# Performance work log

Measured on AMD Instinct MI355X. Metric: run time of the kernel, lower is better.

The kernel has to match this reference:

```python
import jax, jax.numpy as jnp
import numpy as np
from jax import lax

INPUT_SIZE = 512
THRESHOLD = 0.5
IOU_TH = 0.3
MAX_ROIS = 32   # py_cpu_nms(...)[:32]
ROI = 7
NEG = jnp.float32(-1e30)


def _make_anchors(fh, fw, stride):
    # 3 scales x 3 ratios = 9 anchors per cell, laid out in (h, w, anchor)
    # order to match permute(0,2,3,1).view(-1) of the conv heads.
    scales = np.array([32.0, 64.0, 128.0])
    ratios = np.array([0.5, 1.0, 2.0])
    ws = (scales[:, None] * np.sqrt(ratios)[None, :]).reshape(-1)
    hs = (scales[:, None] / np.sqrt(ratios)[None, :]).reshape(-1)
    cy = (np.arange(fh) + 0.5) * stride
    cx = (np.arange(fw) + 0.5) * stride
    CX, CY = np.meshgrid(cx, cy)
    CX = CX[..., None]; CY = CY[..., None]
    a = np.stack([CX - ws / 2, CY - hs / 2, CX + ws / 2, CY + hs / 2], axis=-1)
    return jnp.asarray(a.reshape(-1, 4), jnp.float32)


def setup_inputs() -> dict:
    key = jax.random.key(0)
    k1, k2, k3 = jax.random.split(key, 3)
    B, C, FH, FW, A, stride = 4, 256, 64, 64, 9, 8
    featureMap = jax.random.normal(k1, (B, C, FH, FW), jnp.float32)
    # small init so sigmoid scores spread across threshold and exp(tw) stays sane
    w_cls = jax.random.normal(k2, (A, C, 3, 3), jnp.float32) * 0.05
    w_loc = jax.random.normal(k3, (4 * A, C, 3, 3), jnp.float32) * 0.01
    prior_anchor = _make_anchors(FH, FW, stride)
    return {"featureMap": featureMap, "prior_anchor": prior_anchor,
            "w_cls": w_cls, "w_loc": w_loc, "stride": stride}


def _conv(x, w):
    return lax.conv_general_dilated(x, w, (1, 1), "SAME",
                                    dimension_numbers=("NCHW", "OIHW", "NCHW"))


def _decode(loc, anchors):
    aw = anchors[:, 2] - anchors[:, 0]
    ah = anchors[:, 3] - anchors[:, 1]
    acx = anchors[:, 0] + 0.5 * aw
    acy = anchors[:, 1] + 0.5 * ah
    cx = acx + loc[:, 0] * aw
    cy = acy + loc[:, 1] * ah
    w = aw * jnp.exp(loc[:, 2])
    h = ah * jnp.exp(loc[:, 3])
    return jnp.stack([cx - 0.5 * w, cy - 0.5 * h, cx + 0.5 * w, cy + 0.5 * h], axis=1)


def _iou_one(box, boxes):
    xx1 = jnp.maximum(box[0], boxes[:, 0]); yy1 = jnp.maximum(box[1], boxes[:, 1])
    xx2 = jnp.minimum(box[2], boxes[:, 2]); yy2 = jnp.minimum(box[3], boxes[:, 3])
    inter = jnp.clip(xx2 - xx1, 0) * jnp.clip(yy2 - yy1, 0)
    a1 = (box[2] - box[0]) * (box[3] - box[1])
    a2 = (boxes[:, 2] - boxes[:, 0]) * (boxes[:, 3] - boxes[:, 1])
    return inter / (a1 + a2 - inter + 1e-9)


def _nms(boxes, scores, valid):
    # greedy NMS, fixed MAX_ROIS rounds (== sort-by-score py_cpu_nms + [:32])
    N = scores.shape[0]
    s0 = jnp.where(valid, scores, -1.0)

    def body(i, carry):
        s, picks, ok = carry
        idx = jnp.argmax(s)
        good = s[idx] > 0.0
        picks = picks.at[i].set(idx.astype(jnp.int32))
        ok = ok.at[i].set(good)
        sup = (_iou_one(boxes[idx], boxes) > IOU_TH) | (jnp.arange(N) == idx)
        return (jnp.where(sup, -1.0, s), picks, ok)

    _, picks, ok = lax.fori_loop(
        0, MAX_ROIS, body,
        (s0, jnp.zeros(MAX_ROIS, jnp.int32), jnp.zeros(MAX_ROIS, bool)))
    return picks, ok


def _ceil_div(a, b):
    return -(-a // b)


def _adaptive_maxpool(feat, box):
    # feat: [C, FH, FW]; box: int32 [x1, y1, x2, y2] in feature-map coords.
    # Faithful F.adaptive_max_pool2d bins: start=floor(i*h/7), end=ceil((i+1)*h/7).
    FH, FW = feat.shape[1], feat.shape[2]
    x1, y1, x2, y2 = box[0], box[1], box[2], box[3]
    h = y2 - y1; w = x2 - x1
    i = jnp.arange(ROI)
    rs = y1 + (i * h) // ROI; re = y1 + _ceil_div((i + 1) * h, ROI)
    cs = x1 + (i * w) // ROI; ce = x1 + _ceil_div((i + 1) * w, ROI)
    hh = jnp.arange(FH); ww = jnp.arange(FW)
    rm = jnp.where((hh >= rs[:, None]) & (hh < re[:, None]), 0.0, NEG)  # [7, FH]
    cm = jnp.where((ww >= cs[:, None]) & (ww < ce[:, None]), 0.0, NEG)  # [7, FW]
    t = jnp.max(feat[None] + rm[:, None, :, None], axis=2)              # [7, C, FW]
    out = jnp.max(t[:, None] + cm[None, :, None, :], axis=3)            # [7, 7, C]
    return jnp.transpose(out, (2, 0, 1))                                # [C, 7, 7]


def reference(featureMap, prior_anchor, w_cls, w_loc, stride):
    B, C, FH, FW = featureMap.shape
    cls = jax.nn.sigmoid(_conv(featureMap, w_cls))                      # [B, A, FH, FW]
    cls = jnp.transpose(cls, (0, 2, 3, 1)).reshape(B, -1)               # [B, N]
    loc = jnp.transpose(_conv(featureMap, w_loc), (0, 2, 3, 1)).reshape(B, -1, 4)
    boxes = jax.vmap(_decode, in_axes=(0, None))(loc, prior_anchor)     # [B, N, 4]
    boxes = jnp.clip(boxes, 0.0, float(INPUT_SIZE))                     # clamp(0, input_size)
    valid = (cls > THRESHOLD) \
          & (boxes[..., 2] - boxes[..., 0] >= 2 * stride) \
          & (boxes[..., 3] - boxes[..., 1] >= 2 * stride)
    picks, ok = jax.vmap(_nms)(boxes, cls, valid)                       # [B, 32]
    sel_boxes = jnp.take_along_axis(boxes, picks[..., None], axis=1)    # [B, 32, 4]
    sel_scores = jnp.take_along_axis(cls, picks, axis=1)                # [B, 32]
    eval_boxes = jnp.where(
        ok[..., None],
        jnp.concatenate([sel_boxes, sel_scores[..., None]], axis=-1), 0.0)
    # src_coordinate.int() / stride -> integer feature-map coords
    ib = sel_boxes.astype(jnp.int32) // stride
    fx1 = jnp.clip(ib[..., 0], 0, FW - 1); fy1 = jnp.clip(ib[..., 1], 0, FH - 1)
    fx2 = jnp.clip(ib[..., 2], fx1 + 1, FW); fy2 = jnp.clip(ib[..., 3], fy1 + 1, FH)
    fb = jnp.stack([fx1, fy1, fx2, fy2], axis=-1).reshape(-1, 4)        # [B*32, 4]
    img = jnp.repeat(jnp.arange(B), MAX_ROIS)
    rois = lax.map(lambda a: _adaptive_maxpool(featureMap[a[1]], a[0]), (fb, img))
    rois = jnp.where(ok.reshape(-1)[:, None, None, None], rois, 0.0)    # [B*32, 256, 7, 7]
    return eval_boxes, ok, rois
```

## Files before the change

kernel.cpp:

```cpp
#include <hip/hip_runtime.h>
#include <hip/hip_bf16.h>

#define FHH 64
#define FWW 64
#define CIN 256
#define NB 4
#define NA 9
#define NANCH 36864
#define NPOS 4096
#define OC_TOTAL 45
#define OCP 48
#define MAXROIS 32
#define ROI 7
#define NEGV -1e30f
#define NCHUNK 576
#define NTH 16
#define CAP 1024

typedef unsigned long long u64;

__device__ __constant__ const float TH_LADDER[NTH] = {
    0.9999f, 0.9998f, 0.9995f, 0.999f, 0.998f, 0.997f, 0.995f, 0.993f,
    0.99f, 0.987f, 0.984f, 0.98f, 0.975f, 0.97f, 0.96f, 0.0f};

__global__ __launch_bounds__(256) void wtrans_kernel(
    const float* __restrict__ wcls,
    const float* __restrict__ wloc,
    float* __restrict__ wT,
    int* __restrict__ gcnt)
{
    if (blockIdx.x == 0 && threadIdx.x < NB * NTH) gcnt[threadIdx.x] = 0;
    int idx = blockIdx.x * 256 + threadIdx.x;
    int o = idx % 48;
    int rest = idx / 48;
    int tap = rest % 9;
    int c = rest / 9;
    float v = 0.f;
    if (o < OC_TOTAL) {
        v = (o < NA) ? wcls[((size_t)o * CIN + c) * 9 + tap]
                     : wloc[((size_t)(o - NA) * CIN + c) * 9 + tap];
    }
    wT[idx] = v;
}

__global__ __launch_bounds__(256) void conv_kernel(
    const float* __restrict__ feat,
    const float* __restrict__ wT,
    float* __restrict__ partial,
    int nkg, int cpk)
{
    __shared__ float flds[16][18][20];

    int blk = blockIdx.x;
    int low = blk & 7;
    int rest = blk >> 3;
    int kg = rest % nkg;
    int uhi = rest / nkg;
    int unit = uhi * 8 + low;
    int b = unit >> 4;
    int tile = unit & 15;

    int ty0 = (tile >> 2) * 16;
    int tx0 = (tile & 3) * 16;

    int pb = threadIdx.x & 63;
    int q = __builtin_amdgcn_readfirstlane(threadIdx.x >> 6);
    int ry0 = (pb >> 3) * 2;
    int rx0 = (pb & 7) * 2;

    int cbase = kg * cpk;

    float acc[2][2][12];
#pragma unroll
    for (int py = 0; py < 2; ++py)
#pragma unroll
        for (int px = 0; px < 2; ++px)
#pragma unroll
            for (int o = 0; o < 12; ++o) acc[py][px][o] = 0.f;

    for (int c0 = 0; c0 < cpk; c0 += 16) {
        __syncthreads();
        for (int idx = threadIdx.x; idx < 16 * 324; idx += 256) {
            int c = idx / 324;
            int r = idx - c * 324;
            int y = r / 18;
            int x = r - y * 18;
            int gy = ty0 + y - 1;
            int gx = tx0 + x - 1;
            float v = 0.f;
            if ((unsigned)gy < FHH && (unsigned)gx < FWW)
                v = feat[((size_t)(b * CIN + cbase + c0 + c) * FHH + gy) * FWW + gx];
            flds[c][y][x] = v;
        }
        __syncthreads();

        const float* wq = wT + (size_t)(cbase + c0) * 432 + q * 12;
        for (int c = 0; c < 16; ++c) {
            float f[4][4];
#pragma unroll
            for (int r = 0; r < 4; ++r) {
                float2 a0 = *(const float2*)&flds[c][ry0 + r][rx0];
                float2 a1 = *(const float2*)&flds[c][ry0 + r][rx0 + 2];
                f[r][0] = a0.x; f[r][1] = a0.y; f[r][2] = a1.x; f[r][3] = a1.y;
            }
#pragma unroll
            for (int tap = 0; tap < 9; ++tap) {
                int dy = tap / 3, dx = tap % 3;
                const float* wp = wq + (c * 9 + tap) * 48;
                float w[12];
#pragma unroll
                for (int o = 0; o < 12; ++o) w[o] = wp[o];
#pragma unroll
                for (int py = 0; py < 2; ++py)
#pragma unroll
                for (int px = 0; px < 2; ++px) {
                    float fv = f[py + dy][px + dx];
#pragma unroll
                    for (int o = 0; o < 12; ++o)
                        acc[py][px][o] += fv * w[o];
                }
            }
        }
    }

    float* pout = partial + ((size_t)kg * NB + b) * OCP * NPOS;
#pragma unroll
    for (int o = 0; o < 12; ++o) {
        int oo = q * 12 + o;
        float* op = pout + (size_t)oo * NPOS;
#pragma unroll
        for (int py = 0; py < 2; ++py)
#pragma unroll
        for (int px = 0; px < 2; ++px) {
            int pos = (ty0 + ry0 + py) * FWW + (tx0 + rx0 + px);
            op[pos] = acc[py][px][o];
        }
    }
}

__global__ __launch_bounds__(256) void decode_kernel(
    const float* __restrict__ partial,
    const float* __restrict__ anchors,
    const int* __restrict__ stridep,
    float* __restrict__ boxes,
    float* __restrict__ scores,
    int* __restrict__ gcnt,
    int nkg)
{
    __shared__ int hcnt[NTH];
    if (threadIdx.x < NTH) hcnt[threadIdx.x] = 0;
    __syncthreads();

    int t = blockIdx.x * 256 + threadIdx.x;
    int pos = t & (NPOS - 1);
    int ba = t >> 12;
    int b = ba / 9;
    int a = ba - b * 9;

    float cls = 0.f, l0 = 0.f, l1 = 0.f, l2 = 0.f, l3 = 0.f;
    for (int kg = 0; kg < nkg; ++kg) {
        const float* pk = partial + ((size_t)kg * NB + b) * OCP * NPOS;
        cls += pk[(size_t)a * NPOS + pos];
        l0 += pk[(size_t)(NA + a * 4 + 0) * NPOS + pos];
        l1 += pk[(size_t)(NA + a * 4 + 1) * NPOS + pos];
        l2 += pk[(size_t)(NA + a * 4 + 2) * NPOS + pos];
        l3 += pk[(size_t)(NA + a * 4 + 3) * NPOS + pos];
    }

    float sig = 1.f / (1.f + expf(-cls));
    int n = pos * NA + a;
    const float* an = anchors + (size_t)n * 4;
    float ax1 = an[0], ay1 = an[1], ax2 = an[2], ay2 = an[3];
    float aw = ax2 - ax1, ah = ay2 - ay1;
    float acx = ax1 + 0.5f * aw, acy = ay1 + 0.5f * ah;
    float cx = acx + l0 * aw;
    float cy = acy + l1 * ah;
    float w = aw * expf(l2);
    float h = ah * expf(l3);
    float x1 = fminf(fmaxf(cx - 0.5f * w, 0.f), 512.f);
    float y1 = fminf(fmaxf(cy - 0.5f * h, 0.f), 512.f);
    float x2 = fminf(fmaxf(cx + 0.5f * w, 0.f), 512.f);
    float y2 = fminf(fmaxf(cy + 0.5f * h, 0.f), 512.f);
    int stride = stridep[0];
    float msz = 2.f * (float)stride;
    bool valid = (sig > 0.5f) && ((x2 - x1) >= msz) && ((y2 - y1) >= msz);
    ((float4*)boxes)[(size_t)b * NANCH + n] = make_float4(x1, y1, x2, y2);
    scores[(size_t)b * NANCH + n] = valid ? sig : -1.0f;

#pragma unroll
    for (int i = 0; i < NTH; ++i) {
        u64 mb = __ballot(valid && sig >= TH_LADDER[i]);
        if ((threadIdx.x & 63) == 0 && mb)
            atomicAdd(&hcnt[i], (int)__popcll(mb));
    }
    __syncthreads();
    if (threadIdx.x < NTH && hcnt[threadIdx.x])
        atomicAdd(&gcnt[b * NTH + threadIdx.x], hcnt[threadIdx.x]);
}

__global__ __launch_bounds__(64) void choose_kernel(
    const int* __restrict__ gcnt,
    float* __restrict__ Tsel, int* __restrict__ Csel, int* __restrict__ Vsel,
    int* __restrict__ force, int* __restrict__ gcount, int cap)
{
    int b = threadIdx.x;
    if (b >= NB) return;
    int bestc = 0; float bt = TH_LADDER[0];
    for (int i = 0; i < NTH; ++i) {
        int c = gcnt[b * NTH + i];
        if (c <= cap && c > bestc) { bestc = c; bt = TH_LADDER[i]; }
    }
    int frc = (gcnt[b * NTH + 0] > cap) ? 1 : 0;
    if (frc) { bestc = cap; bt = TH_LADDER[0]; }
    Tsel[b] = bt; Csel[b] = bestc; Vsel[b] = gcnt[b * NTH + NTH - 1];
    force[b] = frc; gcount[b] = 0;
}

__global__ __launch_bounds__(256) void nms_compact_kernel(
    const float* __restrict__ scores,
    const float* __restrict__ Tsel,
    int* __restrict__ gcount,
    u64* __restrict__ candkey,
    int cap)
{
    __shared__ int lcnt;
    __shared__ int wbase[4];
    __shared__ int gbase;
    int t = blockIdx.x * 256 + threadIdx.x;
    int b = t / NANCH;
    int j = t - b * NANCH;
    int lane = threadIdx.x & 63;
    int w = threadIdx.x >> 6;
    if (threadIdx.x == 0) lcnt = 0;
    __syncthreads();
    float v = scores[t];
    float T = Tsel[b];
    bool p = (v > 0.f) && (v >= T);
    u64 m = __ballot(p);
    int cnt = (int)__popcll(m);
    if (lane == 0) wbase[w] = atomicAdd(&lcnt, cnt);
    __syncthreads();
    if (threadIdx.x == 0) gbase = lcnt ? atomicAdd(&gcount[b], lcnt) : 0;
    __syncthreads();
    if (p) {
        int off = (int)__popcll(m & ((1ULL << lane) - 1ULL));
        int slot = gbase + wbase[w] + off;
        if (slot < cap)
            candkey[(size_t)b * cap + slot] =
                ((u64)__float_as_uint(v) << 32) | (unsigned int)(~j);
    }
}

__device__ __forceinline__ void write_outputs(
    int b, int i, bool okv, int idx, float sc,
    const float4* Bb4, const int* stridep,
    float* d_out, int* ifb, int* iok)
{
    float4 bb = Bb4[idx];
    float* eb = d_out + ((size_t)b * MAXROIS + i) * 5;
    eb[0] = okv ? bb.x : 0.f;
    eb[1] = okv ? bb.y : 0.f;
    eb[2] = okv ? bb.z : 0.f;
    eb[3] = okv ? bb.w : 0.f;
    eb[4] = okv ? sc : 0.f;
    d_out[NB * MAXROIS * 5 + b * MAXROIS + i] = okv ? 1.f : 0.f;
    int st = stridep[0];
    int fx1 = min(max(((int)bb.x) / st, 0), FWW - 1);
    int fy1 = min(max(((int)bb.y) / st, 0), FHH - 1);
    int fx2 = min(max(((int)bb.z) / st, fx1 + 1), FWW);
    int fy2 = min(max(((int)bb.w) / st, fy1 + 1), FHH);
    int r = b * MAXROIS + i;
    ifb[r * 4 + 0] = fx1;
    ifb[r * 4 + 1] = fy1;
    ifb[r * 4 + 2] = fx2;
    ifb[r * 4 + 3] = fy2;
    iok[r] = okv ? 1 : 0;
}

__global__ __launch_bounds__(512) void nms_sortscan_kernel(
    const u64* __restrict__ candkey,
    const float* __restrict__ boxes,
    const int* __restrict__ Csel, const int* __restrict__ Vsel,
    const int* __restrict__ force,
    const int* __restrict__ stridep,
    float* __restrict__ d_out,
    int* __restrict__ ifb, int* __restrict__ iok, int* __restrict__ flag,
    int cap)
{
    __shared__ u64 skey[CAP];
    __shared__ float4 box_l[CAP];
    __shared__ u64 mask[CAP / 64];
    __shared__ int picks[MAXROIS];
    __shared__ int np_sh;

    int b = blockIdx.x;
    int tid = threadIdx.x;
    int lane = tid & 63;
    int C = Csel[b];
    if (tid == 0) np_sh = 0;

    int CSZ = 64;
    while (CSZ < C) CSZ <<= 1;

    for (int j = tid; j < CSZ; j += 512)
        skey[j] = (j < C) ? candkey[(size_t)b * cap + j] : 0ULL;

    int prev_cross = 1;
    for (int kk = 2; kk <= CSZ; kk <<= 1) {
        for (int jj = kk >> 1; jj > 0; jj >>= 1) {
            int cross = (jj >= 128) ? 1 : 0;
            if (cross || prev_cross) __syncthreads();
            for (int tt = tid; tt < (CSZ >> 1); tt += 512) {
                int i = ((tt & ~(jj - 1)) << 1) | (tt & (jj - 1));
                int l = i + jj;
                u64 a = skey[i], c2 = skey[l];
                bool up = ((i & kk) == 0);
                bool sw = up ? (a < c2) : (a > c2);
                if (sw) { skey[i] = c2; skey[l] = a; }
            }
            prev_cross = cross;
        }
    }
    __syncthreads();

    const float4* Bb4 = (const float4*)(boxes + (size_t)b * NANCH * 4);
    for (int j = tid; j < C; j += 512) {
        int id = (int)(~((unsigned int)(skey[j] & 0xFFFFFFFFULL)));
        box_l[j] = Bb4[id];
    }
    if (tid < CAP / 64) {
        int base = tid * 64;
        u64 m0;
        if (base >= C) m0 = ~0ULL;
        else if (base + 64 > C) m0 = ~((1ULL << (C - base)) - 1ULL);
        else m0 = 0ULL;
        mask[tid] = m0;
    }
    __syncthreads();

    for (int round = 0; round < MAXROIS; ++round) {
        u64 mw = (lane < CAP / 64) ? mask[lane] : ~0ULL;
        int bpos = __ffsll((u64)(~mw));
        int cand = bpos ? lane * 64 + bpos - 1 : 0x7FFFFFFF;
#pragma unroll
        for (int off = 32; off >= 1; off >>= 1)
            cand = min(cand, __shfl_xor(cand, off));
        int pj = cand;
        if (pj == 0x7FFFFFFF) break;
        if (tid == 0) {
            picks[round] = pj;
            np_sh = round + 1;
            atomicOr(&mask[pj >> 6], 1ULL << (pj & 63));
        }
        float4 pb = box_l[pj];
        float parea = (pb.z - pb.x) * (pb.w - pb.y);
        int j0 = tid * 2;
        u64 curm = mask[tid >> 5];
        u64 addm = 0ULL;
#pragma unroll
        for (int d = 0; d < 2; ++d) {
            int j = j0 + d;
            if (j > pj && j < C && !((curm >> (j & 63)) & 1ULL)) {
                float4 bb2 = box_l[j];
                float xx1 = fmaxf(pb.x, bb2.x), yy1 = fmaxf(pb.y, bb2.y);
                float xx2 = fminf(pb.z, bb2.z), yy2 = fminf(pb.w, bb2.w);
                float inter = fmaxf(xx2 - xx1, 0.f) * fmaxf(yy2 - yy1, 0.f);
                float a2 = (bb2.z - bb2.x) * (bb2.w - bb2.y);
                float iou = inter / (parea + a2 - inter + 1e-9f);
                if (iou > 0.3f) addm |= 1ULL << (j & 63);
            }
        }
        if (addm) atomicOr(&mask[tid >> 5], addm);
        __syncthreads();
    }
    __syncthreads();

    int np = np_sh;
    bool need_fb = force[b] || (np < MAXROIS && Vsel[b] > C);
    if (tid == 0) flag[b] = need_fb ? 1 : 0;
    if (!need_fb && tid < MAXROIS) {
        int i = tid;
        bool okv = i < np;
        int slot = okv ? picks[i] : 0;
        u64 k = skey[slot];
        int idx = okv ? (int)(~((unsigned int)(k & 0xFFFFFFFFULL))) : 0;
        float sc = okv ? __uint_as_float((unsigned int)(k >> 32)) : 0.f;
        write_outputs(b, i, okv, idx, sc, Bb4, stridep, d_out, ifb, iok);
    }
}

__global__ __launch_bounds__(1024) void nms_fallback_kernel(
    const float* __restrict__ boxes,
    const float* __restrict__ scores,
    const int* __restrict__ stridep,
    float* __restrict__ d_out,
    int* __restrict__ ifb,
    int* __restrict__ iok,
    const int* __restrict__ flag)
{
    __shared__ float s[NANCH];
    __shared__ float2 cmax[NCHUNK];
    __shared__ int   picks_sh[MAXROIS];
    __shared__ float pscore_sh[MAXROIS];

    int b = blockIdx.x;
    if (flag[b] == 0) return;

    const float4* Bb4 = (const float4*)(boxes + (size_t)b * NANCH * 4);
    const float* Sb = scores + (size_t)b * NANCH;
    int lane = threadIdx.x & 63;
    int w = threadIdx.x >> 6;

    for (int k = 0; k < 36; ++k) {
        int ch = w * 36 + k;
        int j = ch * 64 + lane;
        float v = Sb[j];
        s[j] = v;
        float bv = v; int bi = j;
#pragma unroll
        for (int off = 32; off >= 1; off >>= 1) {
            float ov = __shfl_xor(bv, off);
            int   oi = __shfl_xor(bi, off);
            if (ov > bv || (ov == bv && oi < bi)) { bv = ov; bi = oi; }
        }
        if (lane == 0) cmax[ch] = make_float2(bv, __int_as_float(bi));
    }
    __syncthreads();
    if (w != 0) return;

    float px1 = 0.f, py1 = 0.f, px2 = 0.f, py2 = 0.f, parea = 0.f;
    int np = 0;
    while (np < MAXROIS) {
        float bv = -2.f; int bi = 0x7fffffff;
#pragma unroll
        for (int k = 0; k < 9; ++k) {
            float2 cm = cmax[lane * 9 + k];
            int ci = __float_as_int(cm.y);
            if (cm.x > bv || (cm.x == bv && ci < bi)) { bv = cm.x; bi = ci; }
        }
#pragma unroll
        for (int off = 32; off >= 1; off >>= 1) {
            float ov = __shfl_xor(bv, off);
            int   oi = __shfl_xor(bi, off);
            if (ov > bv || (ov == bv && oi < bi)) { bv = ov; bi = oi; }
        }
        if (bv <= 0.f) break;
        int fi = bi; float fs = bv;

        float4 cbb = Bb4[fi];

        bool sup = false;
        if (lane < np) {
            float xx1 = fmaxf(px1, cbb.x), yy1 = fmaxf(py1, cbb.y);
            float xx2 = fminf(px2, cbb.z), yy2 = fminf(py2, cbb.w);
            float inter = fmaxf(xx2 - xx1, 0.f) * fmaxf(yy2 - yy1, 0.f);
            float a2 = (cbb.z - cbb.x) * (cbb.w - cbb.y);
            float iou = inter / (parea + a2 - inter + 1e-9f);
            sup = iou > 0.3f;
        }
        u64 m = __ballot(sup);

        int ch = fi >> 6;
        int j = ch * 64 + lane;
        float sv = (j == fi) ? -1.f : s[j];
        if (j == fi) s[j] = -1.f;
        float nv = sv; int ni = j;
#pragma unroll
        for (int off = 32; off >= 1; off >>= 1) {
            float ov = __shfl_xor(nv, off);
            int   oi = __shfl_xor(ni, off);
            if (ov > nv || (ov == nv && oi < ni)) { nv = ov; ni = oi; }
        }
        if (lane == 0) cmax[ch] = make_float2(nv, __int_as_float(ni));

        if (m == 0ULL) {
            if (lane == np) {
                px1 = cbb.x; py1 = cbb.y; px2 = cbb.z; py2 = cbb.w;
                parea = (px2 - px1) * (py2 - py1);
            }
            picks_sh[np] = fi;
            pscore_sh[np] = fs;
            ++np;
        }
    }

    if (lane < MAXROIS) {
        int i = lane;
        bool okv = i < np;
        int idx = okv ? picks_sh[i] : 0;
        float sc = okv ? pscore_sh[i] : 0.f;
        write_outputs(b, i, okv, idx, sc, Bb4, stridep, d_out, ifb, iok);
    }
}

__global__ __launch_bounds__(256) void roi_kernel(
    const float* __restrict__ feat,
    const int* __restrict__ ifb,
    const int* __restrict__ iok,
    float* __restrict__ out_rois)
{
    int t = blockIdx.x * 256 + threadIdx.x;
    int bin = t % 49;
    int rc = t / 49;
    int c = rc & 255;
    int r = rc >> 8;
    int i = bin / 7;
    int j = bin - i * 7;

    if (!iok[r]) { out_rois[t] = 0.f; return; }

    int x1 = ifb[r * 4 + 0];
    int y1 = ifb[r * 4 + 1];
    int x2 = ifb[r * 4 + 2];
    int y2 = ifb[r * 4 + 3];
    int h = y2 - y1;
    int w = x2 - x1;
    int b = r >> 5;

    int rs = y1 + (i * h) / ROI;
    int re = y1 + ((i + 1) * h + ROI - 1) / ROI;
    int cs = x1 + (j * w) / ROI;
    int ce = x1 + ((j + 1) * w + ROI - 1) / ROI;

    const float* F = feat + (size_t)(b * CIN + c) * NPOS;
    float m = NEGV;
    for (int y = rs; y < re; ++y) {
        const float* row = F + y * FWW;
        for (int x = cs; x < ce; ++x) m = fmaxf(m, row[x]);
    }
    out_rois[t] = m;
}

extern "C" void kernel_launch(void* const* d_in, const int* in_sizes, int n_in,
                              void* d_out, int out_size, void* d_ws, size_t ws_size,
                              hipStream_t stream) {
    const float* feat    = (const float*)d_in[0];
    const float* anchors = (const float*)d_in[1];
    const float* wcls    = (const float*)d_in[2];
    const float* wloc    = (const float*)d_in[3];
    const int*   stridep = (const int*)d_in[4];
    float* out = (float*)d_out;
    float* ws  = (float*)d_ws;

    const size_t P1 = (size_t)NB * OCP * NPOS;
    const size_t WTN = 256 * 9 * 48;
    const int cap = CAP;

    auto need = [&](int nk) -> size_t {
        size_t f = P1 * nk
                 + 589824 + 147456 + WTN
                 + (size_t)NB * cap * 2
                 + 2048;
        return f * 4;
    };
    int nkg = 16;
    if (ws_size < need(16)) {
        if (ws_size >= need(8)) { nkg = 8; }
        else { nkg = 4; }
    }

    float* partial   = ws;
    float* boxes     = partial + P1 * nkg;
    float* scores    = boxes + (size_t)NB * NANCH * 4;
    float* wT        = scores + (size_t)NB * NANCH;
    u64*   candkey   = (u64*)(wT + WTN);
    float* tailf     = (float*)(candkey + (size_t)NB * cap);
    int*   ifb       = (int*)tailf;
    int*   iok       = ifb + 512;
    int*   flag      = iok + 128;
    int*   gcnt      = flag + 4;
    float* Tsel      = (float*)(gcnt + 64);
    int*   Csel      = (int*)(Tsel + 4);
    int*   Vsel      = Csel + 4;
    int*   force     = Vsel + 4;
    int*   gcount    = force + 4;

    wtrans_kernel<<<432, 256, 0, stream>>>(wcls, wloc, wT, gcnt);
    conv_kernel<<<64 * nkg, 256, 0, stream>>>(feat, wT, partial, nkg, CIN / nkg);
    decode_kernel<<<(NB * NANCH) / 256, 256, 0, stream>>>(partial, anchors, stridep, boxes, scores, gcnt, nkg);
    choose_kernel<<<1, 64, 0, stream>>>(gcnt, Tsel, Csel, Vsel, force, gcount, cap);
    nms_compact_kernel<<<(NB * NANCH) / 256, 256, 0, stream>>>(scores, Tsel, gcount, candkey, cap);
    nms_sortscan_kernel<<<NB, 512, 0, stream>>>(candkey, boxes, Csel, Vsel, force, stridep, out, ifb, iok, flag, cap);
    nms_fallback_kernel<<<NB, 1024, 0, stream>>>(boxes, scores, stridep, out, ifb, iok, flag);
    roi_kernel<<<(NB * MAXROIS * CIN * 49) / 256, 256, 0, stream>>>(feat, ifb, iok, out + NB * MAXROIS * 5 + NB * MAXROIS);
}
```

Before: 140.1 us.

## Enlarge conv register tile to 2x4 and stage weights in LDS

The conv kernel now gives each thread a 2x4 pixel block (tiles of 16x32 instead of 16x16) and loads 8 channels per stage, with the weight slice for those channels copied into shared memory as float4s instead of read from global memory per tap. Outputs are written with float4 stores. The aim is more FMA per shared and global load and fewer weight fetches, at the cost of more accumulator registers and half as many blocks launched.

```diff
diff --git a/kernel.cpp b/kernel.cpp
--- a/kernel.cpp
+++ b/kernel.cpp
@@ -49,7 +49,8 @@
     float* __restrict__ partial,
     int nkg, int cpk)
 {
-    __shared__ float flds[16][18][20];
+    __shared__ float flds[8][18][40];
+    __shared__ float wlds[8][9][48];
 
     int blk = blockIdx.x;
     int low = blk & 7;
@@ -57,34 +58,33 @@
     int kg = rest % nkg;
     int uhi = rest / nkg;
     int unit = uhi * 8 + low;
-    int b = unit >> 4;
-    int tile = unit & 15;
-
-    int ty0 = (tile >> 2) * 16;
-    int tx0 = (tile & 3) * 16;
-
-    int pb = threadIdx.x & 63;
-    int q = __builtin_amdgcn_readfirstlane(threadIdx.x >> 6);
-    int ry0 = (pb >> 3) * 2;
-    int rx0 = (pb & 7) * 2;
+    int b = unit >> 3;
+    int tile = unit & 7;
+    int ty0 = (tile >> 1) * 16;
+    int tx0 = (tile & 1) * 32;
+
+    int slot = threadIdx.x & 63;
+    int q = threadIdx.x >> 6;
+    int ry0 = (slot >> 3) * 2;
+    int rx0 = (slot & 7) * 4;
 
     int cbase = kg * cpk;
 
-    float acc[2][2][12];
+    float acc[2][4][12];
 #pragma unroll
     for (int py = 0; py < 2; ++py)
 #pragma unroll
-        for (int px = 0; px < 2; ++px)
+        for (int px = 0; px < 4; ++px)
 #pragma unroll
             for (int o = 0; o < 12; ++o) acc[py][px][o] = 0.f;
 
-    for (int c0 = 0; c0 < cpk; c0 += 16) {
+    for (int c0 = 0; c0 < cpk; c0 += 8) {
         __syncthreads();
-        for (int idx = threadIdx.x; idx < 16 * 324; idx += 256) {
-            int c = idx / 324;
-            int r = idx - c * 324;
-            int y = r / 18;
-            int x = r - y * 18;
+        for (int idx = threadIdx.x; idx < 8 * 612; idx += 256) {
+            int c = idx / 612;
+            int r = idx - c * 612;
+            int y = r / 34;
+            int x = r - y * 34;
             int gy = ty0 + y - 1;
             int gx = tx0 + x - 1;
             float v = 0.f;
@@ -92,28 +92,38 @@
                 v = feat[((size_t)(b * CIN + cbase + c0 + c) * FHH + gy) * FWW + gx];
             flds[c][y][x] = v;
         }
+        {
+            const float4* src = (const float4*)(wT + (size_t)(cbase + c0) * 432);
+            float4* dst = (float4*)&wlds[0][0][0];
+            for (int idx = threadIdx.x; idx < 864; idx += 256)
+                dst[idx] = src[idx];
+        }
         __syncthreads();
 
-        const float* wq = wT + (size_t)(cbase + c0) * 432 + q * 12;
-        for (int c = 0; c < 16; ++c) {
-            float f[4][4];
+        for (int c = 0; c < 8; ++c) {
+            float f[4][6];
 #pragma unroll
             for (int r = 0; r < 4; ++r) {
                 float2 a0 = *(const float2*)&flds[c][ry0 + r][rx0];
                 float2 a1 = *(const float2*)&flds[c][ry0 + r][rx0 + 2];
-                f[r][0] = a0.x; f[r][1] = a0.y; f[r][2] = a1.x; f[r][3] = a1.y;
+                float2 a2 = *(const float2*)&flds[c][ry0 + r][rx0 + 4];
+                f[r][0] = a0.x; f[r][1] = a0.y; f[r][2] = a1.x;
+                f[r][3] = a1.y; f[r][4] = a2.x; f[r][5] = a2.y;
             }
 #pragma unroll
             for (int tap = 0; tap < 9; ++tap) {
-                int dy = tap / 3, dx = tap % 3;
-                const float* wp = wq + (c * 9 + tap) * 48;
-                float w[12];
-#pragma unroll
-                for (int o = 0; o < 12; ++o) w[o] = wp[o];
+                const int dy = tap / 3, dx = tap % 3;
+                const float* wp = &wlds[c][tap][q * 12];
+                float4 w0 = *(const float4*)(wp);
+                float4 w1 = *(const float4*)(wp + 4);
+                float4 w2 = *(const float4*)(wp + 8);
+                float w[12] = {w0.x, w0.y, w0.z, w0.w,
+                               w1.x, w1.y, w1.z, w1.w,
+                               w2.x, w2.y, w2.z, w2.w};
 #pragma unroll
                 for (int py = 0; py < 2; ++py)
 #pragma unroll
-                for (int px = 0; px < 2; ++px) {
+                for (int px = 0; px < 4; ++px) {
                     float fv = f[py + dy][px + dx];
 #pragma unroll
                     for (int o = 0; o < 12; ++o)
@@ -129,11 +139,12 @@
         int oo = q * 12 + o;
         float* op = pout + (size_t)oo * NPOS;
 #pragma unroll
-        for (int py = 0; py < 2; ++py)
-#pragma unroll
-        for (int px = 0; px < 2; ++px) {
-            int pos = (ty0 + ry0 + py) * FWW + (tx0 + rx0 + px);
-            op[pos] = acc[py][px][o];
+        for (int py = 0; py < 2; ++py) {
+            int row = ty0 + ry0 + py;
+            int col = tx0 + rx0;
+            float4 v = make_float4(acc[py][0][o], acc[py][1][o],
+                                   acc[py][2][o], acc[py][3][o]);
+            *(float4*)&op[row * FWW + col] = v;
         }
     }
 }
@@ -576,7 +587,7 @@
     int*   gcount    = force + 4;
 
     wtrans_kernel<<<432, 256, 0, stream>>>(wcls, wloc, wT, gcnt);
-    conv_kernel<<<64 * nkg, 256, 0, stream>>>(feat, wT, partial, nkg, CIN / nkg);
+    conv_kernel<<<32 * nkg, 256, 0, stream>>>(feat, wT, partial, nkg, CIN / nkg);
     decode_kernel<<<(NB * NANCH) / 256, 256, 0, stream>>>(partial, anchors, stridep, boxes, scores, gcnt, nkg);
     choose_kernel<<<1, 64, 0, stream>>>(gcnt, Tsel, Csel, Vsel, force, gcount, cap);
     nms_compact_kernel<<<(NB * NANCH) / 256, 256, 0, stream>>>(scores, Tsel, gcount, candkey, cap);
```

Result: slower. 146.4 us (+4.4%).
